# Kernel tuning notes

Measured on AMD Instinct MI355X. Metric: run time of the kernel, lower is better.

The kernel has to match this reference:

```python
import jax, jax.numpy as jnp
import numpy as np

B, D, H, O, E, K = 16384, 128, 512, 128, 8, 2
T = 1.0
EPS = float(np.finfo(float).eps)  # combine() zero-fill epsilon


def cv_squared(v):
    # torch .var() is unbiased (ddof=1)
    return jnp.var(v, ddof=1) / (jnp.mean(v) ** 2 + 1e-10)


def setup_inputs() -> dict:
    key = jax.random.key(0)
    k0, k1, k2, k3, k4, k5 = jax.random.split(key, 6)
    x = jax.random.normal(k0, (B, D), dtype=jnp.float32)
    w_gate = jax.random.normal(k1, (D, E), dtype=jnp.float32) * 0.02
    w1 = jax.random.normal(k2, (E, D, H), dtype=jnp.float32) * (1.0 / np.sqrt(D))
    b1 = jax.random.normal(k3, (E, H), dtype=jnp.float32) * 0.01
    w2 = jax.random.normal(k4, (E, H, O), dtype=jnp.float32) * (1.0 / np.sqrt(H))
    b2 = jax.random.normal(k5, (E, O), dtype=jnp.float32) * 0.01
    return {"x": x, "w_gate": w_gate, "w1": w1, "b1": b1, "w2": w2, "b2": b2}


def reference(x, w_gate, w1, b1, w2, b2):
    # ---- noisy top-k gating (eval mode: clean logits, no noise) ----
    logits = x @ w_gate                                   # [B, E]
    top_logits, top_idx = jax.lax.top_k(logits, K)        # [B, K]
    top_gates = jax.nn.softmax(top_logits / T, axis=-1)   # [B, K]
    gates = jnp.zeros_like(logits).at[jnp.arange(x.shape[0])[:, None], top_idx].set(top_gates)

    importance = gates.sum(0)                              # [E]
    load = (gates > 0).sum(0).astype(jnp.float32)          # [E]
    loss = cv_squared(importance) + cv_squared(load)

    # ---- experts (dense gate-weighted form of dispatch/combine) ----
    # output[b] = Sum_i gates[b,i] * expert_i(x[b]); zero gates contribute nothing,
    # identical math to SparseDispatcher's gather / per-expert MLP / scatter-add.
    h = jax.nn.relu(jnp.einsum('bd,edh->beh', x, w1) + b1[None])   # [B, E, H]
    y_e = jnp.einsum('beh,eho->beo', h, w2) + b2[None]             # [B, E, O]
    y = jnp.einsum('be,beo->bo', gates, y_e)                       # [B, O]
    # combine(): combined[combined == 0] = eps
    y = jnp.where(y == 0, jnp.asarray(EPS, y.dtype), y)
    return y, loss
```

## Files before the change

### kernel.cpp

```cpp
#include <hip/hip_runtime.h>
#include <hip/hip_bf16.h>
#include <math.h>

#define NB 16384
#define ND 128
#define NH 512
#define NO 128
#define NE 8
#define NCH 16
#define EPSF 2.2204460492503131e-16f

using bf16x8 = __attribute__((ext_vector_type(8))) short;
using f32x16 = __attribute__((ext_vector_type(16))) float;
using uint2v = __attribute__((ext_vector_type(2))) unsigned;

#define WS_BLKCNT 0u
#define WS_BLKIMP 8192u
#define WS_TOKID  16384u
#define WS_TOKGG  1064960u
#define WS_XBF    1196032u
#define WS_W1F    5390336u
#define WS_W2F    6438912u
#define WS_YSTAGE 7487488u

__device__ __forceinline__ unsigned f2bf(float f){
  unsigned u = __float_as_uint(f);
  u += 0x7FFFu + ((u >> 16) & 1u);
  return u >> 16;
}
__device__ __forceinline__ unsigned cvtpk(float lo, float hi){
  unsigned r;
  asm("v_cvt_pk_bf16_f32 %0, %1, %2" : "=v"(r) : "v"(lo), "v"(hi));
  return r;
}
__device__ __forceinline__ void gld16(const void* g, void* l){
  __builtin_amdgcn_global_load_lds((const __attribute__((address_space(1))) void*)g,
                                   (__attribute__((address_space(3))) void*)l, 16, 0, 0);
}

__global__ __launch_bounds__(256) void prep_kernel(
    const float* __restrict__ x, const float* __restrict__ wg,
    const float* __restrict__ w1, const float* __restrict__ w2,
    unsigned short* __restrict__ xbf, unsigned short* __restrict__ w1f,
    unsigned short* __restrict__ w2f, int* __restrict__ blk_cnt,
    float* __restrict__ blk_imp, int* __restrict__ tok_ids, float2* __restrict__ tok_gg){
  int bx = blockIdx.x, tid = threadIdx.x;
  if (bx >= 512){
    int u = (bx - 512)*256 + tid;
    int o = u & 127, hb = (u>>7)&3, c = (u>>9)&15, e = u>>13;
    int h0 = c*32 + (hb>>1)*16 + (hb&1)*8;
    const float* src = w2 + (size_t)e*NH*NO + (size_t)h0*NO + o;
    unsigned q[4];
    #pragma unroll
    for (int p = 0; p < 4; ++p)
      q[p] = f2bf(src[(2*p)*NO]) | (f2bf(src[(2*p+1)*NO]) << 16);
    *(uint4*)(w2f + (size_t)u*8) = make_uint4(q[0], q[1], q[2], q[3]);
    return;
  }
  if (bx >= 256){
    int u = (bx - 256)*256 + tid;
    int h32 = u & 31, db = (u>>5)&15, c = (u>>9)&15, e = u>>13;
    int d0 = (db>>1)*16 + (db&1)*8;
    int hg = c*32 + h32;
    const float* src = w1 + (size_t)e*ND*NH + (size_t)d0*NH + hg;
    unsigned q[4];
    #pragma unroll
    for (int p = 0; p < 4; ++p)
      q[p] = f2bf(src[(2*p)*NH]) | (f2bf(src[(2*p+1)*NH]) << 16);
    *(uint4*)(w1f + (size_t)u*8) = make_uint4(q[0], q[1], q[2], q[3]);
    return;
  }
  __shared__ int   lcnt[NE];
  __shared__ float limp[NE];
  if (tid < NE){ lcnt[tid] = 0; limp[tid] = 0.f; }
  __syncthreads();
  int tok  = bx*64 + (tid >> 2);
  int part = tid & 3;
  const float4* xr4 = (const float4*)(x + (size_t)tok*ND);
  double acc[NE];
  #pragma unroll
  for (int e = 0; e < NE; ++e) acc[e] = 0.0;
  #pragma unroll
  for (int j = 0; j < 8; ++j){
    int f4 = part + j*4;
    float4 v = xr4[f4];
    uint2 p;
    p.x = f2bf(v.x) | (f2bf(v.y) << 16);
    p.y = f2bf(v.z) | (f2bf(v.w) << 16);
    *(uint2*)(xbf + (size_t)tok*ND + f4*4) = p;
    const float4* wr = (const float4*)(wg + f4*32);
    float vm[4] = {v.x, v.y, v.z, v.w};
    #pragma unroll
    for (int m = 0; m < 4; ++m){
      float4 wa = wr[2*m], wb = wr[2*m+1];
      double d = (double)vm[m];
      acc[0] += d*(double)wa.x; acc[1] += d*(double)wa.y;
      acc[2] += d*(double)wa.z; acc[3] += d*(double)wa.w;
      acc[4] += d*(double)wb.x; acc[5] += d*(double)wb.y;
      acc[6] += d*(double)wb.z; acc[7] += d*(double)wb.w;
    }
  }
  #pragma unroll
  for (int e = 0; e < NE; ++e){
    acc[e] += __shfl_xor(acc[e], 1);
    acc[e] += __shfl_xor(acc[e], 2);
  }
  if (part == 0){
    int i0 = 0;
    double l0 = acc[0];
    #pragma unroll
    for (int e = 1; e < NE; ++e) if (acc[e] > l0){ l0 = acc[e]; i0 = e; }
    int i1 = (i0 == 0) ? 1 : 0;
    double l1 = acc[i1];
    #pragma unroll
    for (int e = 0; e < NE; ++e) if (e != i0 && acc[e] > l1){ l1 = acc[e]; i1 = e; }
    float e1 = expf((float)(l1 - l0));
    float g0 = 1.0f/(1.0f + e1);
    float g1 = e1/(1.0f + e1);
    int s0 = atomicAdd(&lcnt[i0], 1);
    int s1 = atomicAdd(&lcnt[i1], 1);
    atomicAdd(&limp[i0], g0);
    atomicAdd(&limp[i1], g1);
    tok_gg[tok] = make_float2(g0, g1);
    tok_ids[i0*32768 + bx*128 + s0] = tok;
    tok_ids[i1*32768 + bx*128 + s1] = tok | (1 << 30);
  }
  __syncthreads();
  if (tid < NE){
    blk_cnt[bx*8 + tid] = lcnt[tid];
    blk_imp[bx*8 + tid] = limp[tid];
  }
}

__global__ __launch_bounds__(256) void expert_kernel(
    const unsigned short* __restrict__ xbf, const unsigned short* __restrict__ w1f,
    const unsigned short* __restrict__ w2f, const float* __restrict__ b1,
    const float* __restrict__ b2, const int* __restrict__ blk_cnt,
    const int* __restrict__ tok_ids, const float2* __restrict__ tok_gg,
    unsigned short* __restrict__ ystage){
  __shared__ char L[44032];
  int* cnt_l  = (int*)(L + 32768);
  int* gp     = (int*)(L + 40960);
  int* totl   = (int*)(L + 41984);
  int* tbase  = (int*)(L + 42016);
  int* sl_tok = (int*)(L + 42056);
  int tid = threadIdx.x;
  {
    int4 a = *(const int4*)(blk_cnt + tid*8);
    int4 c = *(const int4*)(blk_cnt + tid*8 + 4);
    cnt_l[0*256+tid]=a.x; cnt_l[1*256+tid]=a.y; cnt_l[2*256+tid]=a.z; cnt_l[3*256+tid]=a.w;
    cnt_l[4*256+tid]=c.x; cnt_l[5*256+tid]=c.y; cnt_l[6*256+tid]=c.z; cnt_l[7*256+tid]=c.w;
  }
  __syncthreads();
  {
    int e8 = tid >> 5, g8 = tid & 31;
    int s8 = 0;
    #pragma unroll
    for (int i = 0; i < 8; ++i) s8 += cnt_l[e8*256 + g8*8 + i];
    gp[tid] = s8;
    __syncthreads();
    #pragma unroll
    for (int st = 1; st < 32; st <<= 1){
      int add = (g8 >= st) ? gp[tid - st] : 0;
      __syncthreads();
      gp[tid] += add;
      __syncthreads();
    }
    if (g8 == 31) totl[e8] = gp[tid];
    __syncthreads();
    if (tid == 0){
      tbase[0] = 0;
      #pragma unroll
      for (int e = 0; e < NE; ++e) tbase[e+1] = tbase[e] + ((totl[e] + 127) >> 7);
    }
    __syncthreads();
  }
  int b = blockIdx.x;
  if (b >= tbase[8]) return;
  int e = 0;
  #pragma unroll
  for (int ee = 1; ee < NE; ++ee) if (tbase[ee] <= b) e = ee;
  int n_e  = totl[e];
  int base = (b - tbase[e])*128;
  if (tid < 128){
    int s = base + tid;
    if (s >= n_e) s = n_e - 1;
    int g = 0;
    #pragma unroll
    for (int st = 16; st; st >>= 1){
      int c = g + st;
      if (c <= 31 && gp[e*32 + c - 1] <= s) g = c;
    }
    int acc2 = g ? gp[e*32 + g - 1] : 0;
    int gb = g*8;
    while (true){
      int c2 = cnt_l[e*256 + gb];
      if (acc2 + c2 > s) break;
      acc2 += c2; ++gb;
    }
    sl_tok[tid] = tok_ids[e*32768 + gb*128 + (s - acc2)];
  }
  __syncthreads();

  int wid = tid >> 6, lane = tid & 63, l31 = lane & 31, hi = lane >> 5;
  char* w1buf = L;
  char* w2buf = L + 16384;
  const char* g1base = (const char*)w1f + (size_t)e*131072;
  const char* g2base = (const char*)w2f + (size_t)e*131072;

  int raw0 = sl_tok[wid*32 + l31];
  int tok0 = raw0 & 0x3FFFFFFF;
  bf16x8 xfrag[8];
  #pragma unroll
  for (int k = 0; k < 8; ++k)
    xfrag[k] = *(const bf16x8*)(xbf + (size_t)tok0*ND + (k*2 + hi)*8);

#define STAGE(c, bsel) do { \
    const char* _g1 = g1base + (size_t)(c)*8192 + wid*1024 + lane*16; \
    const char* _g2 = g2base + (size_t)(c)*8192 + wid*1024 + lane*16; \
    char* _l1 = w1buf + (bsel)*8192 + wid*1024; \
    char* _l2 = w2buf + (bsel)*8192 + wid*1024; \
    _Pragma("unroll") \
    for (int _s = 0; _s < 2; ++_s){ \
      gld16(_g1 + _s*4096, _l1 + _s*4096); \
      gld16(_g2 + _s*4096, _l2 + _s*4096); \
    } \
  } while(0)

  STAGE(0, 0);
  f32x16 yacc[4];
  #pragma unroll
  for (int ot = 0; ot < 4; ++ot)
    #pragma unroll
    for (int i = 0; i < 16; ++i) yacc[ot][i] = 0.f;
  __syncthreads();

  for (int c = 0; c < NCH; ++c){
    int bb = c & 1;
    if (c + 1 < NCH) STAGE(c + 1, bb ^ 1);
    f32x16 hacc;
    #pragma unroll
    for (int i = 0; i < 16; ++i) hacc[i] = 0.f;
    #pragma unroll
    for (int k = 0; k < 8; ++k){
      bf16x8 a = *(const bf16x8*)(w1buf + bb*8192 + (k*2 + hi)*512 + l31*16);
      hacc = __builtin_amdgcn_mfma_f32_32x32x16_bf16(a, xfrag[k], hacc, 0, 0, 0);
    }
    const float4* b1p = (const float4*)(b1 + e*NH + c*32 + hi*4);
    float dv[16];
    #pragma unroll
    for (int g = 0; g < 4; ++g){
      float4 bv = b1p[2*g];
      dv[4*g+0] = fmaxf(hacc[4*g+0] + bv.x, 0.f);
      dv[4*g+1] = fmaxf(hacc[4*g+1] + bv.y, 0.f);
      dv[4*g+2] = fmaxf(hacc[4*g+2] + bv.z, 0.f);
      dv[4*g+3] = fmaxf(hacc[4*g+3] + bv.w, 0.f);
    }
    unsigned A0 = cvtpk(dv[0], dv[1]),   A1 = cvtpk(dv[2], dv[3]);
    unsigned A2 = cvtpk(dv[4], dv[5]),   A3 = cvtpk(dv[6], dv[7]);
    unsigned A4 = cvtpk(dv[8], dv[9]),   A5 = cvtpk(dv[10], dv[11]);
    unsigned A6 = cvtpk(dv[12], dv[13]), A7 = cvtpk(dv[14], dv[15]);
    uint2v r0 = __builtin_amdgcn_permlane32_swap(A0, A2, false, false);
    uint2v r1 = __builtin_amdgcn_permlane32_swap(A1, A3, false, false);
    uint2v r2 = __builtin_amdgcn_permlane32_swap(A4, A6, false, false);
    uint2v r3 = __builtin_amdgcn_permlane32_swap(A5, A7, false, false);
    union { unsigned u[4]; bf16x8 v; } fa, fb;
    fa.u[0] = r0[0]; fa.u[1] = r1[0]; fa.u[2] = r0[1]; fa.u[3] = r1[1];
    fb.u[0] = r2[0]; fb.u[1] = r3[0]; fb.u[2] = r2[1]; fb.u[3] = r3[1];
    bf16x8 aht0 = fa.v, aht1 = fb.v;
    #pragma unroll
    for (int ot = 0; ot < 4; ++ot){
      bf16x8 bf0 = *(const bf16x8*)(w2buf + bb*8192 + hi*2048 + (ot*32 + l31)*16);
      yacc[ot] = __builtin_amdgcn_mfma_f32_32x32x16_bf16(aht0, bf0, yacc[ot], 0, 0, 0);
      bf16x8 bf1 = *(const bf16x8*)(w2buf + bb*8192 + (2 + hi)*2048 + (ot*32 + l31)*16);
      yacc[ot] = __builtin_amdgcn_mfma_f32_32x32x16_bf16(aht1, bf1, yacc[ot], 0, 0, 0);
    }
    __syncthreads();
  }
#undef STAGE
  float b2v[4];
  #pragma unroll
  for (int ot = 0; ot < 4; ++ot) b2v[ot] = b2[e*NO + ot*32 + l31];
  #pragma unroll
  for (int r = 0; r < 16; ++r){
    int row = (r & 3) + 8*(r >> 2) + 4*hi;
    int slot = base + wid*32 + row;
    if (slot < n_e){
      int rw = sl_tok[wid*32 + row];
      int tk = rw & 0x3FFFFFFF, wh = (rw >> 30) & 1;
      float2 gg = tok_gg[tk];
      float g = wh ? gg.y : gg.x;
      unsigned short* dst = ystage + ((size_t)tk*2 + wh)*NO + l31;
      #pragma unroll
      for (int ot = 0; ot < 4; ++ot)
        dst[ot*32] = (unsigned short)f2bf((yacc[ot][r] + b2v[ot]) * g);
    }
  }
}

__global__ __launch_bounds__(256) void combine_kernel(
    const unsigned short* __restrict__ ystage, const int* __restrict__ blk_cnt,
    const float* __restrict__ blk_imp, float* __restrict__ y){
  if (blockIdx.x == 0){
    __shared__ int   scnt[32];
    __shared__ float simp[32];
    int tid = threadIdx.x, lane = tid & 63, wid = tid >> 6;
    int4 ca = *(const int4*)(blk_cnt + tid*8);
    int4 cb = *(const int4*)(blk_cnt + tid*8 + 4);
    float4 ia = *(const float4*)(blk_imp + tid*8);
    float4 ib = *(const float4*)(blk_imp + tid*8 + 4);
    int   cv[8] = {ca.x, ca.y, ca.z, ca.w, cb.x, cb.y, cb.z, cb.w};
    float iv[8] = {ia.x, ia.y, ia.z, ia.w, ib.x, ib.y, ib.z, ib.w};
    #pragma unroll
    for (int e = 0; e < NE; ++e){
      int   rc = cv[e];
      float ri = iv[e];
      #pragma unroll
      for (int st = 1; st < 64; st <<= 1){
        rc += __shfl_xor(rc, st);
        ri += __shfl_xor(ri, st);
      }
      if (lane == 0){ scnt[e*4 + wid] = rc; simp[e*4 + wid] = ri; }
    }
    __syncthreads();
    if (tid == 0){
      double si = 0, sqi = 0, sl = 0, sql = 0;
      #pragma unroll
      for (int e = 0; e < NE; ++e){
        double a = (double)(simp[e*4] + simp[e*4+1] + simp[e*4+2] + simp[e*4+3]);
        double bb = (double)(scnt[e*4] + scnt[e*4+1] + scnt[e*4+2] + scnt[e*4+3]);
        si += a; sqi += a*a; sl += bb; sql += bb*bb;
      }
      double mi = si/8.0, vi = (sqi - 8.0*mi*mi)/7.0;
      double ml = sl/8.0, vl = (sql - 8.0*ml*ml)/7.0;
      y[NB*NO] = (float)(vi/(mi*mi + 1e-10) + vl/(ml*ml + 1e-10));
    }
  }
  int idx = blockIdx.x*256 + threadIdx.x;
  int tk = idx >> 4, q = idx & 15;
  const unsigned short* r0 = ystage + (size_t)tk*256 + q*8;
  uint4 a = *(const uint4*)r0;
  uint4 bq = *(const uint4*)(r0 + 128);
  unsigned aw[4] = {a.x, a.y, a.z, a.w};
  unsigned bw[4] = {bq.x, bq.y, bq.z, bq.w};
  float outs[8];
  #pragma unroll
  for (int i = 0; i < 4; ++i){
    float vlo = __uint_as_float(aw[i] << 16)         + __uint_as_float(bw[i] << 16);
    float vhi = __uint_as_float(aw[i] & 0xFFFF0000u) + __uint_as_float(bw[i] & 0xFFFF0000u);
    outs[2*i]   = (vlo == 0.f) ? EPSF : vlo;
    outs[2*i+1] = (vhi == 0.f) ? EPSF : vhi;
  }
  float4 o0 = {outs[0], outs[1], outs[2], outs[3]};
  float4 o1 = {outs[4], outs[5], outs[6], outs[7]};
  float* dst = y + (size_t)tk*128 + q*8;
  *(float4*)dst     = o0;
  *(float4*)(dst+4) = o1;
}

extern "C" void kernel_launch(void* const* d_in, const int* in_sizes, int n_in,
                              void* d_out, int out_size, void* d_ws, size_t ws_size,
                              hipStream_t stream){
  (void)in_sizes; (void)n_in; (void)out_size; (void)ws_size;
  const float* x  = (const float*)d_in[0];
  const float* wg = (const float*)d_in[1];
  const float* w1 = (const float*)d_in[2];
  const float* b1 = (const float*)d_in[3];
  const float* w2 = (const float*)d_in[4];
  const float* b2 = (const float*)d_in[5];
  float* out = (float*)d_out;
  char* ws = (char*)d_ws;
  int*            blk_cnt = (int*)(ws + WS_BLKCNT);
  float*          blk_imp = (float*)(ws + WS_BLKIMP);
  int*            tok_ids = (int*)(ws + WS_TOKID);
  float2*         tok_gg  = (float2*)(ws + WS_TOKGG);
  unsigned short* xbf     = (unsigned short*)(ws + WS_XBF);
  unsigned short* w1f     = (unsigned short*)(ws + WS_W1F);
  unsigned short* w2f     = (unsigned short*)(ws + WS_W2F);
  unsigned short* ystage  = (unsigned short*)(ws + WS_YSTAGE);

  prep_kernel<<<768, 256, 0, stream>>>(x, wg, w1, w2, xbf, w1f, w2f,
                                       blk_cnt, blk_imp, tok_ids, tok_gg);
  expert_kernel<<<264, 256, 0, stream>>>(xbf, w1f, w2f, b1, b2,
                                         blk_cnt, tok_ids, tok_gg, ystage);
  combine_kernel<<<1024, 256, 0, stream>>>(ystage, blk_cnt, blk_imp, out);
}
```

Baseline: 48.39 us.

## Fuse combine into expert kernel via float atomicAdd into pre-zeroed output

Removes the separate combine kernel and the bf16 staging buffer. The prep kernel now zeroes the output, and the expert kernel atomically adds each gate-weighted expert result straight into the fp32 output. The expert kernel's block 0 also computes the load-balancing loss. This saves one launch and the staging write and read, at the cost of global atomic traffic and an extra zeroing pass. The order of the two per-token additions is now nondeterministic, and the epsilon substitution for exact-zero outputs is dropped.

```diff
diff --git a/kernel.cpp b/kernel.cpp
--- a/kernel.cpp
+++ b/kernel.cpp
@@ -21,7 +21,6 @@
 #define WS_XBF    1196032u
 #define WS_W1F    5390336u
 #define WS_W2F    6438912u
-#define WS_YSTAGE 7487488u
 
 __device__ __forceinline__ unsigned f2bf(float f){
   unsigned u = __float_as_uint(f);
@@ -43,7 +42,8 @@
     const float* __restrict__ w1, const float* __restrict__ w2,
     unsigned short* __restrict__ xbf, unsigned short* __restrict__ w1f,
     unsigned short* __restrict__ w2f, int* __restrict__ blk_cnt,
-    float* __restrict__ blk_imp, int* __restrict__ tok_ids, float2* __restrict__ tok_gg){
+    float* __restrict__ blk_imp, int* __restrict__ tok_ids, float2* __restrict__ tok_gg,
+    float* __restrict__ y){
   int bx = blockIdx.x, tid = threadIdx.x;
   if (bx >= 512){
     int u = (bx - 512)*256 + tid;
@@ -69,6 +69,13 @@
       q[p] = f2bf(src[(2*p)*NH]) | (f2bf(src[(2*p+1)*NH]) << 16);
     *(uint4*)(w1f + (size_t)u*8) = make_uint4(q[0], q[1], q[2], q[3]);
     return;
+  }
+  {
+    float4 z = {0.f, 0.f, 0.f, 0.f};
+    float* yb = y + (size_t)bx*64*NO + tid*32;
+    #pragma unroll
+    for (int i = 0; i < 8; ++i) *(float4*)(yb + i*4) = z;
+    if (bx == 0 && tid == 0) y[NB*NO] = 0.f;
   }
   __shared__ int   lcnt[NE];
   __shared__ float limp[NE];
@@ -136,14 +143,15 @@
     const unsigned short* __restrict__ xbf, const unsigned short* __restrict__ w1f,
     const unsigned short* __restrict__ w2f, const float* __restrict__ b1,
     const float* __restrict__ b2, const int* __restrict__ blk_cnt,
-    const int* __restrict__ tok_ids, const float2* __restrict__ tok_gg,
-    unsigned short* __restrict__ ystage){
+    const float* __restrict__ blk_imp, const int* __restrict__ tok_ids,
+    const float2* __restrict__ tok_gg, float* __restrict__ y){
   __shared__ char L[44032];
   int* cnt_l  = (int*)(L + 32768);
   int* gp     = (int*)(L + 40960);
   int* totl   = (int*)(L + 41984);
   int* tbase  = (int*)(L + 42016);
   int* sl_tok = (int*)(L + 42056);
+  float* simp = (float*)(L + 42568);
   int tid = threadIdx.x;
   {
     int4 a = *(const int4*)(blk_cnt + tid*8);
@@ -177,6 +185,32 @@
   }
   int b = blockIdx.x;
   if (b >= tbase[8]) return;
+  if (b == 0){
+    int lane = tid & 63, wv = tid >> 6;
+    float4 ia = *(const float4*)(blk_imp + tid*8);
+    float4 ib = *(const float4*)(blk_imp + tid*8 + 4);
+    float iv[8] = {ia.x, ia.y, ia.z, ia.w, ib.x, ib.y, ib.z, ib.w};
+    #pragma unroll
+    for (int e2 = 0; e2 < NE; ++e2){
+      float ri = iv[e2];
+      #pragma unroll
+      for (int st = 1; st < 64; st <<= 1) ri += __shfl_xor(ri, st);
+      if (lane == 0) simp[e2*4 + wv] = ri;
+    }
+    __syncthreads();
+    if (tid == 0){
+      double si = 0, sqi = 0, sl = 0, sql = 0;
+      #pragma unroll
+      for (int e2 = 0; e2 < NE; ++e2){
+        double a = (double)(simp[e2*4] + simp[e2*4+1] + simp[e2*4+2] + simp[e2*4+3]);
+        double bb = (double)totl[e2];
+        si += a; sqi += a*a; sl += bb; sql += bb*bb;
+      }
+      double mi = si/8.0, vi = (sqi - 8.0*mi*mi)/7.0;
+      double ml = sl/8.0, vl = (sql - 8.0*ml*ml)/7.0;
+      y[NB*NO] = (float)(vi/(mi*mi + 1e-10) + vl/(ml*ml + 1e-10));
+    }
+  }
   int e = 0;
   #pragma unroll
   for (int ee = 1; ee < NE; ++ee) if (tbase[ee] <= b) e = ee;
@@ -290,72 +324,12 @@
       int tk = rw & 0x3FFFFFFF, wh = (rw >> 30) & 1;
       float2 gg = tok_gg[tk];
       float g = wh ? gg.y : gg.x;
-      unsigned short* dst = ystage + ((size_t)tk*2 + wh)*NO + l31;
+      float* yrow = y + (size_t)tk*NO + l31;
       #pragma unroll
       for (int ot = 0; ot < 4; ++ot)
-        dst[ot*32] = (unsigned short)f2bf((yacc[ot][r] + b2v[ot]) * g);
-    }
-  }
-}
-
-__global__ __launch_bounds__(256) void combine_kernel(
-    const unsigned short* __restrict__ ystage, const int* __restrict__ blk_cnt,
-    const float* __restrict__ blk_imp, float* __restrict__ y){
-  if (blockIdx.x == 0){
-    __shared__ int   scnt[32];
-    __shared__ float simp[32];
-    int tid = threadIdx.x, lane = tid & 63, wid = tid >> 6;
-    int4 ca = *(const int4*)(blk_cnt + tid*8);
-    int4 cb = *(const int4*)(blk_cnt + tid*8 + 4);
-    float4 ia = *(const float4*)(blk_imp + tid*8);
-    float4 ib = *(const float4*)(blk_imp + tid*8 + 4);
-    int   cv[8] = {ca.x, ca.y, ca.z, ca.w, cb.x, cb.y, cb.z, cb.w};
-    float iv[8] = {ia.x, ia.y, ia.z, ia.w, ib.x, ib.y, ib.z, ib.w};
-    #pragma unroll
-    for (int e = 0; e < NE; ++e){
-      int   rc = cv[e];
-      float ri = iv[e];
-      #pragma unroll
-      for (int st = 1; st < 64; st <<= 1){
-        rc += __shfl_xor(rc, st);
-        ri += __shfl_xor(ri, st);
-      }
-      if (lane == 0){ scnt[e*4 + wid] = rc; simp[e*4 + wid] = ri; }
-    }
-    __syncthreads();
-    if (tid == 0){
-      double si = 0, sqi = 0, sl = 0, sql = 0;
-      #pragma unroll
-      for (int e = 0; e < NE; ++e){
-        double a = (double)(simp[e*4] + simp[e*4+1] + simp[e*4+2] + simp[e*4+3]);
-        double bb = (double)(scnt[e*4] + scnt[e*4+1] + scnt[e*4+2] + scnt[e*4+3]);
-        si += a; sqi += a*a; sl += bb; sql += bb*bb;
-      }
-      double mi = si/8.0, vi = (sqi - 8.0*mi*mi)/7.0;
-      double ml = sl/8.0, vl = (sql - 8.0*ml*ml)/7.0;
-      y[NB*NO] = (float)(vi/(mi*mi + 1e-10) + vl/(ml*ml + 1e-10));
-    }
-  }
-  int idx = blockIdx.x*256 + threadIdx.x;
-  int tk = idx >> 4, q = idx & 15;
-  const unsigned short* r0 = ystage + (size_t)tk*256 + q*8;
-  uint4 a = *(const uint4*)r0;
-  uint4 bq = *(const uint4*)(r0 + 128);
-  unsigned aw[4] = {a.x, a.y, a.z, a.w};
-  unsigned bw[4] = {bq.x, bq.y, bq.z, bq.w};
-  float outs[8];
-  #pragma unroll
-  for (int i = 0; i < 4; ++i){
-    float vlo = __uint_as_float(aw[i] << 16)         + __uint_as_float(bw[i] << 16);
-    float vhi = __uint_as_float(aw[i] & 0xFFFF0000u) + __uint_as_float(bw[i] & 0xFFFF0000u);
-    outs[2*i]   = (vlo == 0.f) ? EPSF : vlo;
-    outs[2*i+1] = (vhi == 0.f) ? EPSF : vhi;
-  }
-  float4 o0 = {outs[0], outs[1], outs[2], outs[3]};
-  float4 o1 = {outs[4], outs[5], outs[6], outs[7]};
-  float* dst = y + (size_t)tk*128 + q*8;
-  *(float4*)dst     = o0;
-  *(float4*)(dst+4) = o1;
+        atomicAdd(yrow + ot*32, (yacc[ot][r] + b2v[ot]) * g);
+    }
+  }
 }
 
 extern "C" void kernel_launch(void* const* d_in, const int* in_sizes, int n_in,
@@ -377,11 +351,9 @@
   unsigned short* xbf     = (unsigned short*)(ws + WS_XBF);
   unsigned short* w1f     = (unsigned short*)(ws + WS_W1F);
   unsigned short* w2f     = (unsigned short*)(ws + WS_W2F);
-  unsigned short* ystage  = (unsigned short*)(ws + WS_YSTAGE);
 
   prep_kernel<<<768, 256, 0, stream>>>(x, wg, w1, w2, xbf, w1f, w2f,
-                                       blk_cnt, blk_imp, tok_ids, tok_gg);
+                                       blk_cnt, blk_imp, tok_ids, tok_gg, out);
   expert_kernel<<<264, 256, 0, stream>>>(xbf, w1f, w2f, b1, b2,
-                                         blk_cnt, tok_ids, tok_gg, ystage);
-  combine_kernel<<<1024, 256, 0, stream>>>(ystage, blk_cnt, blk_imp, out);
-}
+                                         blk_cnt, blk_imp, tok_ids, tok_gg, out);
+}
```

Measured after the change: 53.80 us. 11.2% more time.

## Restructure expert kernel into single-wave 64-token blocks with barrier-free pipelining

Applied to the files above, without the earlier changes.

Each expert block becomes a single 64-lane wavefront that handles 64 tokens as two 32-token MFMA groups sharing every weight fragment. The prefix-scan switches from shared-memory scans with block barriers to wave shuffles, and the weight chunks move through a two-deep prefetch controlled by explicit vmcnt waits instead of __syncthreads. b1 is staged in LDS. The launch grows to 520 small blocks, which raises the block count but lowers waves per block. Each wave also stages the full weight set itself, so per-wave load traffic goes up.

```diff
diff --git a/kernel.cpp b/kernel.cpp
--- a/kernel.cpp
+++ b/kernel.cpp
@@ -7,7 +7,6 @@
 #define NH 512
 #define NO 128
 #define NE 8
-#define NCH 16
 #define EPSF 2.2204460492503131e-16f
 
 using bf16x8 = __attribute__((ext_vector_type(8))) short;
@@ -132,58 +131,62 @@
   }
 }
 
-__global__ __launch_bounds__(256) void expert_kernel(
+__global__ __launch_bounds__(64, 1) void expert_kernel(
     const unsigned short* __restrict__ xbf, const unsigned short* __restrict__ w1f,
     const unsigned short* __restrict__ w2f, const float* __restrict__ b1,
     const float* __restrict__ b2, const int* __restrict__ blk_cnt,
     const int* __restrict__ tok_ids, const float2* __restrict__ tok_gg,
     unsigned short* __restrict__ ystage){
-  __shared__ char L[44032];
-  int* cnt_l  = (int*)(L + 32768);
-  int* gp     = (int*)(L + 40960);
-  int* totl   = (int*)(L + 41984);
-  int* tbase  = (int*)(L + 42016);
-  int* sl_tok = (int*)(L + 42056);
-  int tid = threadIdx.x;
-  {
-    int4 a = *(const int4*)(blk_cnt + tid*8);
-    int4 c = *(const int4*)(blk_cnt + tid*8 + 4);
-    cnt_l[0*256+tid]=a.x; cnt_l[1*256+tid]=a.y; cnt_l[2*256+tid]=a.z; cnt_l[3*256+tid]=a.w;
-    cnt_l[4*256+tid]=c.x; cnt_l[5*256+tid]=c.y; cnt_l[6*256+tid]=c.z; cnt_l[7*256+tid]=c.w;
-  }
-  __syncthreads();
-  {
-    int e8 = tid >> 5, g8 = tid & 31;
+  __shared__ char L[35200];
+  char*  wbuf   = L;
+  int*   cnt_l  = (int*)L;
+  int*   gp     = (int*)(L + 8192);
+  int*   sl_tok = (int*)(L + 32768);
+  float* b1s    = (float*)(L + 33024);
+  int*   totl   = (int*)(L + 35072);
+  int*   tbase  = (int*)(L + 35104);
+  int lane = threadIdx.x, l31 = lane & 31, hi = lane >> 5;
+
+  #pragma unroll
+  for (int j = 0; j < 4; ++j){
+    int blk = lane + j*64;
+    int4 a = *(const int4*)(blk_cnt + blk*8);
+    int4 c4 = *(const int4*)(blk_cnt + blk*8 + 4);
+    cnt_l[0*256+blk]=a.x;  cnt_l[1*256+blk]=a.y;  cnt_l[2*256+blk]=a.z;  cnt_l[3*256+blk]=a.w;
+    cnt_l[4*256+blk]=c4.x; cnt_l[5*256+blk]=c4.y; cnt_l[6*256+blk]=c4.z; cnt_l[7*256+blk]=c4.w;
+  }
+  asm volatile("s_waitcnt lgkmcnt(0)" ::: "memory");
+  #pragma unroll
+  for (int p = 0; p < 4; ++p){
+    int e8 = p*2 + hi, g = l31;
     int s8 = 0;
     #pragma unroll
-    for (int i = 0; i < 8; ++i) s8 += cnt_l[e8*256 + g8*8 + i];
-    gp[tid] = s8;
-    __syncthreads();
+    for (int i = 0; i < 8; ++i) s8 += cnt_l[e8*256 + g*8 + i];
+    int pre = s8;
     #pragma unroll
     for (int st = 1; st < 32; st <<= 1){
-      int add = (g8 >= st) ? gp[tid - st] : 0;
-      __syncthreads();
-      gp[tid] += add;
-      __syncthreads();
-    }
-    if (g8 == 31) totl[e8] = gp[tid];
-    __syncthreads();
-    if (tid == 0){
-      tbase[0] = 0;
-      #pragma unroll
-      for (int e = 0; e < NE; ++e) tbase[e+1] = tbase[e] + ((totl[e] + 127) >> 7);
-    }
-    __syncthreads();
-  }
+      int o = __shfl_up(pre, st, 32);
+      if (g >= st) pre += o;
+    }
+    gp[e8*32 + g] = pre;
+    if (g == 31) totl[e8] = pre;
+  }
+  asm volatile("s_waitcnt lgkmcnt(0)" ::: "memory");
+  if (lane == 0){
+    tbase[0] = 0;
+    #pragma unroll
+    for (int e = 0; e < NE; ++e) tbase[e+1] = tbase[e] + ((totl[e] + 63) >> 6);
+  }
+  asm volatile("s_waitcnt lgkmcnt(0)" ::: "memory");
   int b = blockIdx.x;
   if (b >= tbase[8]) return;
   int e = 0;
   #pragma unroll
   for (int ee = 1; ee < NE; ++ee) if (tbase[ee] <= b) e = ee;
   int n_e  = totl[e];
-  int base = (b - tbase[e])*128;
-  if (tid < 128){
-    int s = base + tid;
+  int base = (b - tbase[e])*64;
+  {
+    int s = base + lane;
     if (s >= n_e) s = n_e - 1;
     int g = 0;
     #pragma unroll
@@ -198,104 +201,130 @@
       if (acc2 + c2 > s) break;
       acc2 += c2; ++gb;
     }
-    sl_tok[tid] = tok_ids[e*32768 + gb*128 + (s - acc2)];
-  }
-  __syncthreads();
-
-  int wid = tid >> 6, lane = tid & 63, l31 = lane & 31, hi = lane >> 5;
-  char* w1buf = L;
-  char* w2buf = L + 16384;
+    sl_tok[lane] = tok_ids[e*32768 + gb*128 + (s - acc2)];
+  }
+  asm volatile("s_waitcnt lgkmcnt(0)" ::: "memory");
+  gld16((const char*)(b1 + e*NH) + lane*16, b1s);
+  gld16((const char*)(b1 + e*NH) + 1024 + lane*16, (char*)b1s + 1024);
+  int tokA = sl_tok[l31] & 0x3FFFFFFF;
+  int tokB = sl_tok[32 + l31] & 0x3FFFFFFF;
+  bf16x8 xfA[8], xfB[8];
+  #pragma unroll
+  for (int k = 0; k < 8; ++k){
+    xfA[k] = *(const bf16x8*)(xbf + (size_t)tokA*ND + (k*2 + hi)*8);
+    xfB[k] = *(const bf16x8*)(xbf + (size_t)tokB*ND + (k*2 + hi)*8);
+  }
   const char* g1base = (const char*)w1f + (size_t)e*131072;
   const char* g2base = (const char*)w2f + (size_t)e*131072;
 
-  int raw0 = sl_tok[wid*32 + l31];
-  int tok0 = raw0 & 0x3FFFFFFF;
-  bf16x8 xfrag[8];
-  #pragma unroll
-  for (int k = 0; k < 8; ++k)
-    xfrag[k] = *(const bf16x8*)(xbf + (size_t)tok0*ND + (k*2 + hi)*8);
-
 #define STAGE(c, bsel) do { \
-    const char* _g1 = g1base + (size_t)(c)*8192 + wid*1024 + lane*16; \
-    const char* _g2 = g2base + (size_t)(c)*8192 + wid*1024 + lane*16; \
-    char* _l1 = w1buf + (bsel)*8192 + wid*1024; \
-    char* _l2 = w2buf + (bsel)*8192 + wid*1024; \
+    const char* _g1 = g1base + (size_t)(c)*8192 + lane*16; \
+    const char* _g2 = g2base + (size_t)(c)*8192 + lane*16; \
+    char* _l1 = wbuf + (bsel)*16384; \
+    char* _l2 = wbuf + (bsel)*16384 + 8192; \
     _Pragma("unroll") \
-    for (int _s = 0; _s < 2; ++_s){ \
-      gld16(_g1 + _s*4096, _l1 + _s*4096); \
-      gld16(_g2 + _s*4096, _l2 + _s*4096); \
+    for (int _i = 0; _i < 8; ++_i){ \
+      gld16(_g1 + _i*1024, _l1 + _i*1024); \
+      gld16(_g2 + _i*1024, _l2 + _i*1024); \
     } \
   } while(0)
 
+#define REPACK(dv, out0, out1) do { \
+    unsigned A0=cvtpk(dv[0],dv[1]),   A1=cvtpk(dv[2],dv[3]); \
+    unsigned A2=cvtpk(dv[4],dv[5]),   A3=cvtpk(dv[6],dv[7]); \
+    unsigned A4=cvtpk(dv[8],dv[9]),   A5=cvtpk(dv[10],dv[11]); \
+    unsigned A6=cvtpk(dv[12],dv[13]), A7=cvtpk(dv[14],dv[15]); \
+    uint2v r0 = __builtin_amdgcn_permlane32_swap(A0, A2, false, false); \
+    uint2v r1 = __builtin_amdgcn_permlane32_swap(A1, A3, false, false); \
+    uint2v r2 = __builtin_amdgcn_permlane32_swap(A4, A6, false, false); \
+    uint2v r3 = __builtin_amdgcn_permlane32_swap(A5, A7, false, false); \
+    union { unsigned u[4]; bf16x8 v; } fa, fb; \
+    fa.u[0]=r0[0]; fa.u[1]=r1[0]; fa.u[2]=r0[1]; fa.u[3]=r1[1]; \
+    fb.u[0]=r2[0]; fb.u[1]=r3[0]; fb.u[2]=r2[1]; fb.u[3]=r3[1]; \
+    out0 = fa.v; out1 = fb.v; \
+  } while(0)
+
   STAGE(0, 0);
-  f32x16 yacc[4];
+  STAGE(1, 1);
+  f32x16 yA[4], yB[4];
   #pragma unroll
   for (int ot = 0; ot < 4; ++ot)
     #pragma unroll
-    for (int i = 0; i < 16; ++i) yacc[ot][i] = 0.f;
-  __syncthreads();
-
-  for (int c = 0; c < NCH; ++c){
-    int bb = c & 1;
-    if (c + 1 < NCH) STAGE(c + 1, bb ^ 1);
-    f32x16 hacc;
-    #pragma unroll
-    for (int i = 0; i < 16; ++i) hacc[i] = 0.f;
+    for (int i = 0; i < 16; ++i){ yA[ot][i] = 0.f; yB[ot][i] = 0.f; }
+
+  #pragma unroll
+  for (int c = 0; c < 16; ++c){
+    if (c < 14) asm volatile("s_waitcnt vmcnt(16)" ::: "memory");
+    else        asm volatile("s_waitcnt vmcnt(0)"  ::: "memory");
+    __builtin_amdgcn_sched_barrier(0);
+    const char* w1c = wbuf + (c & 1)*16384;
+    const char* w2c = wbuf + (c & 1)*16384 + 8192;
+    f32x16 hA, hB;
+    #pragma unroll
+    for (int i = 0; i < 16; ++i){ hA[i] = 0.f; hB[i] = 0.f; }
     #pragma unroll
     for (int k = 0; k < 8; ++k){
-      bf16x8 a = *(const bf16x8*)(w1buf + bb*8192 + (k*2 + hi)*512 + l31*16);
-      hacc = __builtin_amdgcn_mfma_f32_32x32x16_bf16(a, xfrag[k], hacc, 0, 0, 0);
-    }
-    const float4* b1p = (const float4*)(b1 + e*NH + c*32 + hi*4);
-    float dv[16];
+      bf16x8 a = *(const bf16x8*)(w1c + (k*2 + hi)*512 + l31*16);
+      hA = __builtin_amdgcn_mfma_f32_32x32x16_bf16(a, xfA[k], hA, 0, 0, 0);
+      hB = __builtin_amdgcn_mfma_f32_32x32x16_bf16(a, xfB[k], hB, 0, 0, 0);
+    }
+    float dvA[16], dvB[16];
     #pragma unroll
     for (int g = 0; g < 4; ++g){
-      float4 bv = b1p[2*g];
-      dv[4*g+0] = fmaxf(hacc[4*g+0] + bv.x, 0.f);
-      dv[4*g+1] = fmaxf(hacc[4*g+1] + bv.y, 0.f);
-      dv[4*g+2] = fmaxf(hacc[4*g+2] + bv.z, 0.f);
-      dv[4*g+3] = fmaxf(hacc[4*g+3] + bv.w, 0.f);
-    }
-    unsigned A0 = cvtpk(dv[0], dv[1]),   A1 = cvtpk(dv[2], dv[3]);
-    unsigned A2 = cvtpk(dv[4], dv[5]),   A3 = cvtpk(dv[6], dv[7]);
-    unsigned A4 = cvtpk(dv[8], dv[9]),   A5 = cvtpk(dv[10], dv[11]);
-    unsigned A6 = cvtpk(dv[12], dv[13]), A7 = cvtpk(dv[14], dv[15]);
-    uint2v r0 = __builtin_amdgcn_permlane32_swap(A0, A2, false, false);
-    uint2v r1 = __builtin_amdgcn_permlane32_swap(A1, A3, false, false);
-    uint2v r2 = __builtin_amdgcn_permlane32_swap(A4, A6, false, false);
-    uint2v r3 = __builtin_amdgcn_permlane32_swap(A5, A7, false, false);
-    union { unsigned u[4]; bf16x8 v; } fa, fb;
-    fa.u[0] = r0[0]; fa.u[1] = r1[0]; fa.u[2] = r0[1]; fa.u[3] = r1[1];
-    fb.u[0] = r2[0]; fb.u[1] = r3[0]; fb.u[2] = r2[1]; fb.u[3] = r3[1];
-    bf16x8 aht0 = fa.v, aht1 = fb.v;
+      float4 bv = *(const float4*)(b1s + c*32 + hi*4 + g*8);
+      dvA[4*g+0] = fmaxf(hA[4*g+0] + bv.x, 0.f);
+      dvA[4*g+1] = fmaxf(hA[4*g+1] + bv.y, 0.f);
+      dvA[4*g+2] = fmaxf(hA[4*g+2] + bv.z, 0.f);
+      dvA[4*g+3] = fmaxf(hA[4*g+3] + bv.w, 0.f);
+      dvB[4*g+0] = fmaxf(hB[4*g+0] + bv.x, 0.f);
+      dvB[4*g+1] = fmaxf(hB[4*g+1] + bv.y, 0.f);
+      dvB[4*g+2] = fmaxf(hB[4*g+2] + bv.z, 0.f);
+      dvB[4*g+3] = fmaxf(hB[4*g+3] + bv.w, 0.f);
+    }
+    bf16x8 ahA0, ahA1, ahB0, ahB1;
+    REPACK(dvA, ahA0, ahA1);
+    REPACK(dvB, ahB0, ahB1);
     #pragma unroll
     for (int ot = 0; ot < 4; ++ot){
-      bf16x8 bf0 = *(const bf16x8*)(w2buf + bb*8192 + hi*2048 + (ot*32 + l31)*16);
-      yacc[ot] = __builtin_amdgcn_mfma_f32_32x32x16_bf16(aht0, bf0, yacc[ot], 0, 0, 0);
-      bf16x8 bf1 = *(const bf16x8*)(w2buf + bb*8192 + (2 + hi)*2048 + (ot*32 + l31)*16);
-      yacc[ot] = __builtin_amdgcn_mfma_f32_32x32x16_bf16(aht1, bf1, yacc[ot], 0, 0, 0);
-    }
-    __syncthreads();
+      bf16x8 bf0 = *(const bf16x8*)(w2c + hi*2048 + (ot*32 + l31)*16);
+      bf16x8 bf1 = *(const bf16x8*)(w2c + (2 + hi)*2048 + (ot*32 + l31)*16);
+      yA[ot] = __builtin_amdgcn_mfma_f32_32x32x16_bf16(ahA0, bf0, yA[ot], 0, 0, 0);
+      yA[ot] = __builtin_amdgcn_mfma_f32_32x32x16_bf16(ahA1, bf1, yA[ot], 0, 0, 0);
+      yB[ot] = __builtin_amdgcn_mfma_f32_32x32x16_bf16(ahB0, bf0, yB[ot], 0, 0, 0);
+      yB[ot] = __builtin_amdgcn_mfma_f32_32x32x16_bf16(ahB1, bf1, yB[ot], 0, 0, 0);
+    }
+    if (c + 2 < 16){
+      asm volatile("s_waitcnt lgkmcnt(0)" ::: "memory");
+      __builtin_amdgcn_sched_barrier(0);
+      STAGE(c + 2, c & 1);
+    }
   }
 #undef STAGE
+#undef REPACK
+
   float b2v[4];
   #pragma unroll
   for (int ot = 0; ot < 4; ++ot) b2v[ot] = b2[e*NO + ot*32 + l31];
-  #pragma unroll
-  for (int r = 0; r < 16; ++r){
-    int row = (r & 3) + 8*(r >> 2) + 4*hi;
-    int slot = base + wid*32 + row;
-    if (slot < n_e){
-      int rw = sl_tok[wid*32 + row];
-      int tk = rw & 0x3FFFFFFF, wh = (rw >> 30) & 1;
-      float2 gg = tok_gg[tk];
-      float g = wh ? gg.y : gg.x;
-      unsigned short* dst = ystage + ((size_t)tk*2 + wh)*NO + l31;
-      #pragma unroll
-      for (int ot = 0; ot < 4; ++ot)
-        dst[ot*32] = (unsigned short)f2bf((yacc[ot][r] + b2v[ot]) * g);
-    }
-  }
+#define EPI(G, Y) do { \
+    _Pragma("unroll") \
+    for (int r = 0; r < 16; ++r){ \
+      int row = (r & 3) + 8*(r >> 2) + 4*hi; \
+      int slot = base + (G)*32 + row; \
+      if (slot < n_e){ \
+        int rw = sl_tok[(G)*32 + row]; \
+        int tk = rw & 0x3FFFFFFF, wh = (rw >> 30) & 1; \
+        float2 gg = tok_gg[tk]; \
+        float gsc = wh ? gg.y : gg.x; \
+        unsigned short* dst = ystage + ((size_t)tk*2 + wh)*NO + l31; \
+        _Pragma("unroll") \
+        for (int ot = 0; ot < 4; ++ot) \
+          dst[ot*32] = (unsigned short)f2bf((Y[ot][r] + b2v[ot]) * gsc); \
+      } \
+    } \
+  } while(0)
+  EPI(0, yA);
+  EPI(1, yB);
+#undef EPI
 }
 
 __global__ __launch_bounds__(256) void combine_kernel(
@@ -381,7 +410,7 @@
 
   prep_kernel<<<768, 256, 0, stream>>>(x, wg, w1, w2, xbf, w1f, w2f,
                                        blk_cnt, blk_imp, tok_ids, tok_gg);
-  expert_kernel<<<264, 256, 0, stream>>>(xbf, w1f, w2f, b1, b2,
-                                         blk_cnt, tok_ids, tok_gg, ystage);
+  expert_kernel<<<520, 64, 0, stream>>>(xbf, w1f, w2f, b1, b2,
+                                        blk_cnt, tok_ids, tok_gg, ystage);
   combine_kernel<<<1024, 256, 0, stream>>>(ystage, blk_cnt, blk_imp, out);
 }
```

Result: slower. 56.01 us (+15.8%).

## Split expert MLP over hidden-dim quarters and output halves with more blocks

Applied to the files above, without the earlier changes.

The expert kernel now splits each 64-token tile across 4 blocks, one per quarter of the hidden dimension, and splits each block's warps over two token halves and two output halves. Weights are read straight from global memory instead of being double-buffered through LDS, and the LDS-barrier prefix scan becomes a wave shuffle scan. Each block writes a bf16 partial, with the bias pre-scaled by 0.25, and combine sums 8 partials per token. This targets poor occupancy from only 264 blocks, but it adds extra partial-sum traffic and more bf16 rounding error.

```diff
diff --git a/kernel.cpp b/kernel.cpp
--- a/kernel.cpp
+++ b/kernel.cpp
@@ -7,7 +7,6 @@
 #define NH 512
 #define NO 128
 #define NE 8
-#define NCH 16
 #define EPSF 2.2204460492503131e-16f
 
 using bf16x8 = __attribute__((ext_vector_type(8))) short;
@@ -21,7 +20,7 @@
 #define WS_XBF    1196032u
 #define WS_W1F    5390336u
 #define WS_W2F    6438912u
-#define WS_YSTAGE 7487488u
+#define WS_YST4   7487488u
 
 __device__ __forceinline__ unsigned f2bf(float f){
   unsigned u = __float_as_uint(f);
@@ -32,10 +31,6 @@
   unsigned r;
   asm("v_cvt_pk_bf16_f32 %0, %1, %2" : "=v"(r) : "v"(lo), "v"(hi));
   return r;
-}
-__device__ __forceinline__ void gld16(const void* g, void* l){
-  __builtin_amdgcn_global_load_lds((const __attribute__((address_space(1))) void*)g,
-                                   (__attribute__((address_space(3))) void*)l, 16, 0, 0);
 }
 
 __global__ __launch_bounds__(256) void prep_kernel(
@@ -132,24 +127,22 @@
   }
 }
 
-__global__ __launch_bounds__(256) void expert_kernel(
+__global__ __launch_bounds__(256, 4) void expert_kernel(
     const unsigned short* __restrict__ xbf, const unsigned short* __restrict__ w1f,
     const unsigned short* __restrict__ w2f, const float* __restrict__ b1,
     const float* __restrict__ b2, const int* __restrict__ blk_cnt,
     const int* __restrict__ tok_ids, const float2* __restrict__ tok_gg,
     unsigned short* __restrict__ ystage){
-  __shared__ char L[44032];
-  int* cnt_l  = (int*)(L + 32768);
-  int* gp     = (int*)(L + 40960);
-  int* totl   = (int*)(L + 41984);
-  int* tbase  = (int*)(L + 42016);
-  int* sl_tok = (int*)(L + 42056);
+  __shared__ int cnt_l[NE*256];
+  __shared__ int gp[256];
+  __shared__ int totl[NE];
+  __shared__ int sl_tok[64];
   int tid = threadIdx.x;
   {
     int4 a = *(const int4*)(blk_cnt + tid*8);
-    int4 c = *(const int4*)(blk_cnt + tid*8 + 4);
-    cnt_l[0*256+tid]=a.x; cnt_l[1*256+tid]=a.y; cnt_l[2*256+tid]=a.z; cnt_l[3*256+tid]=a.w;
-    cnt_l[4*256+tid]=c.x; cnt_l[5*256+tid]=c.y; cnt_l[6*256+tid]=c.z; cnt_l[7*256+tid]=c.w;
+    int4 c4 = *(const int4*)(blk_cnt + tid*8 + 4);
+    cnt_l[0*256+tid]=a.x;  cnt_l[1*256+tid]=a.y;  cnt_l[2*256+tid]=a.z;  cnt_l[3*256+tid]=a.w;
+    cnt_l[4*256+tid]=c4.x; cnt_l[5*256+tid]=c4.y; cnt_l[6*256+tid]=c4.z; cnt_l[7*256+tid]=c4.w;
   }
   __syncthreads();
   {
@@ -157,33 +150,32 @@
     int s8 = 0;
     #pragma unroll
     for (int i = 0; i < 8; ++i) s8 += cnt_l[e8*256 + g8*8 + i];
-    gp[tid] = s8;
-    __syncthreads();
+    int pre = s8;
     #pragma unroll
     for (int st = 1; st < 32; st <<= 1){
-      int add = (g8 >= st) ? gp[tid - st] : 0;
-      __syncthreads();
-      gp[tid] += add;
-      __syncthreads();
-    }
-    if (g8 == 31) totl[e8] = gp[tid];
-    __syncthreads();
-    if (tid == 0){
-      tbase[0] = 0;
-      #pragma unroll
-      for (int e = 0; e < NE; ++e) tbase[e+1] = tbase[e] + ((totl[e] + 127) >> 7);
-    }
-    __syncthreads();
-  }
-  int b = blockIdx.x;
-  if (b >= tbase[8]) return;
+      int o = __shfl_up(pre, st, 32);
+      if (g8 >= st) pre += o;
+    }
+    gp[tid] = pre;
+    if (g8 == 31) totl[e8] = pre;
+  }
+  __syncthreads();
+  int tb[9];
+  tb[0] = 0;
+  #pragma unroll
+  for (int e2 = 0; e2 < NE; ++e2) tb[e2+1] = tb[e2] + ((totl[e2] + 63) >> 6);
+  int tile_g = blockIdx.x >> 2, q = blockIdx.x & 3;
+  if (tile_g >= tb[8]) return;
   int e = 0;
   #pragma unroll
-  for (int ee = 1; ee < NE; ++ee) if (tbase[ee] <= b) e = ee;
+  for (int ee = 1; ee < NE; ++ee) if (tb[ee] <= tile_g) e = ee;
   int n_e  = totl[e];
-  int base = (b - tbase[e])*128;
-  if (tid < 128){
-    int s = base + tid;
+  int base = (tile_g - tb[e])*64;
+  int lane = tid & 63, wid = tid >> 6, l31 = lane & 31, hi = lane >> 5;
+  int t = wid & 1, oh = wid >> 1;
+  int raw;
+  {
+    int s = base + t*32 + l31;
     if (s >= n_e) s = n_e - 1;
     int g = 0;
     #pragma unroll
@@ -198,55 +190,39 @@
       if (acc2 + c2 > s) break;
       acc2 += c2; ++gb;
     }
-    sl_tok[tid] = tok_ids[e*32768 + gb*128 + (s - acc2)];
-  }
-  __syncthreads();
-
-  int wid = tid >> 6, lane = tid & 63, l31 = lane & 31, hi = lane >> 5;
-  char* w1buf = L;
-  char* w2buf = L + 16384;
-  const char* g1base = (const char*)w1f + (size_t)e*131072;
-  const char* g2base = (const char*)w2f + (size_t)e*131072;
-
-  int raw0 = sl_tok[wid*32 + l31];
-  int tok0 = raw0 & 0x3FFFFFFF;
-  bf16x8 xfrag[8];
+    raw = tok_ids[e*32768 + gb*128 + (s - acc2)];
+  }
+  if (oh == 0) sl_tok[t*32 + l31] = raw;
+  __syncthreads();
+
+  int tok0 = raw & 0x3FFFFFFF;
+  bf16x8 xf[8];
   #pragma unroll
   for (int k = 0; k < 8; ++k)
-    xfrag[k] = *(const bf16x8*)(xbf + (size_t)tok0*ND + (k*2 + hi)*8);
-
-#define STAGE(c, bsel) do { \
-    const char* _g1 = g1base + (size_t)(c)*8192 + wid*1024 + lane*16; \
-    const char* _g2 = g2base + (size_t)(c)*8192 + wid*1024 + lane*16; \
-    char* _l1 = w1buf + (bsel)*8192 + wid*1024; \
-    char* _l2 = w2buf + (bsel)*8192 + wid*1024; \
-    _Pragma("unroll") \
-    for (int _s = 0; _s < 2; ++_s){ \
-      gld16(_g1 + _s*4096, _l1 + _s*4096); \
-      gld16(_g2 + _s*4096, _l2 + _s*4096); \
-    } \
-  } while(0)
-
-  STAGE(0, 0);
-  f32x16 yacc[4];
-  #pragma unroll
-  for (int ot = 0; ot < 4; ++ot)
+    xf[k] = *(const bf16x8*)(xbf + (size_t)tok0*ND + (k*2 + hi)*8);
+  const char* w1e = (const char*)w1f + (size_t)e*131072;
+  const char* w2e = (const char*)w2f + (size_t)e*131072;
+
+  f32x16 yacc[2];
+  #pragma unroll
+  for (int ot = 0; ot < 2; ++ot)
     #pragma unroll
     for (int i = 0; i < 16; ++i) yacc[ot][i] = 0.f;
-  __syncthreads();
-
-  for (int c = 0; c < NCH; ++c){
-    int bb = c & 1;
-    if (c + 1 < NCH) STAGE(c + 1, bb ^ 1);
+
+  #pragma unroll
+  for (int c = 0; c < 4; ++c){
+    int c32 = q*4 + c;
+    const char* w1c = w1e + (size_t)c32*8192;
+    const char* w2c = w2e + (size_t)c32*8192;
     f32x16 hacc;
     #pragma unroll
     for (int i = 0; i < 16; ++i) hacc[i] = 0.f;
     #pragma unroll
     for (int k = 0; k < 8; ++k){
-      bf16x8 a = *(const bf16x8*)(w1buf + bb*8192 + (k*2 + hi)*512 + l31*16);
-      hacc = __builtin_amdgcn_mfma_f32_32x32x16_bf16(a, xfrag[k], hacc, 0, 0, 0);
-    }
-    const float4* b1p = (const float4*)(b1 + e*NH + c*32 + hi*4);
+      bf16x8 a = *(const bf16x8*)(w1c + (k*2 + hi)*512 + l31*16);
+      hacc = __builtin_amdgcn_mfma_f32_32x32x16_bf16(a, xf[k], hacc, 0, 0, 0);
+    }
+    const float4* b1p = (const float4*)(b1 + e*NH + c32*32 + hi*4);
     float dv[16];
     #pragma unroll
     for (int g = 0; g < 4; ++g){
@@ -269,31 +245,32 @@
     fb.u[0] = r2[0]; fb.u[1] = r3[0]; fb.u[2] = r2[1]; fb.u[3] = r3[1];
     bf16x8 aht0 = fa.v, aht1 = fb.v;
     #pragma unroll
-    for (int ot = 0; ot < 4; ++ot){
-      bf16x8 bf0 = *(const bf16x8*)(w2buf + bb*8192 + hi*2048 + (ot*32 + l31)*16);
+    for (int ot = 0; ot < 2; ++ot){
+      int oidx = ((oh*2 + ot)*32 + l31)*16;
+      bf16x8 bf0 = *(const bf16x8*)(w2c + hi*2048 + oidx);
+      bf16x8 bf1 = *(const bf16x8*)(w2c + (2 + hi)*2048 + oidx);
       yacc[ot] = __builtin_amdgcn_mfma_f32_32x32x16_bf16(aht0, bf0, yacc[ot], 0, 0, 0);
-      bf16x8 bf1 = *(const bf16x8*)(w2buf + bb*8192 + (2 + hi)*2048 + (ot*32 + l31)*16);
       yacc[ot] = __builtin_amdgcn_mfma_f32_32x32x16_bf16(aht1, bf1, yacc[ot], 0, 0, 0);
     }
-    __syncthreads();
-  }
-#undef STAGE
-  float b2v[4];
-  #pragma unroll
-  for (int ot = 0; ot < 4; ++ot) b2v[ot] = b2[e*NO + ot*32 + l31];
+  }
+
+  float b2q = 0.25f;
+  float b2v[2];
+  #pragma unroll
+  for (int ot = 0; ot < 2; ++ot) b2v[ot] = b2[e*NO + (oh*2 + ot)*32 + l31]*b2q;
   #pragma unroll
   for (int r = 0; r < 16; ++r){
     int row = (r & 3) + 8*(r >> 2) + 4*hi;
-    int slot = base + wid*32 + row;
+    int slot = base + t*32 + row;
     if (slot < n_e){
-      int rw = sl_tok[wid*32 + row];
+      int rw = sl_tok[t*32 + row];
       int tk = rw & 0x3FFFFFFF, wh = (rw >> 30) & 1;
       float2 gg = tok_gg[tk];
-      float g = wh ? gg.y : gg.x;
-      unsigned short* dst = ystage + ((size_t)tk*2 + wh)*NO + l31;
+      float gsc = wh ? gg.y : gg.x;
+      unsigned short* dst = ystage + (((size_t)tk*2 + wh)*4 + q)*NO + l31;
       #pragma unroll
-      for (int ot = 0; ot < 4; ++ot)
-        dst[ot*32] = (unsigned short)f2bf((yacc[ot][r] + b2v[ot]) * g);
+      for (int ot = 0; ot < 2; ++ot)
+        dst[(oh*2 + ot)*32] = (unsigned short)f2bf((yacc[ot][r] + b2v[ot]) * gsc);
     }
   }
 }
@@ -337,23 +314,24 @@
     }
   }
   int idx = blockIdx.x*256 + threadIdx.x;
-  int tk = idx >> 4, q = idx & 15;
-  const unsigned short* r0 = ystage + (size_t)tk*256 + q*8;
-  uint4 a = *(const uint4*)r0;
-  uint4 bq = *(const uint4*)(r0 + 128);
-  unsigned aw[4] = {a.x, a.y, a.z, a.w};
-  unsigned bw[4] = {bq.x, bq.y, bq.z, bq.w};
-  float outs[8];
-  #pragma unroll
-  for (int i = 0; i < 4; ++i){
-    float vlo = __uint_as_float(aw[i] << 16)         + __uint_as_float(bw[i] << 16);
-    float vhi = __uint_as_float(aw[i] & 0xFFFF0000u) + __uint_as_float(bw[i] & 0xFFFF0000u);
-    outs[2*i]   = (vlo == 0.f) ? EPSF : vlo;
-    outs[2*i+1] = (vhi == 0.f) ? EPSF : vhi;
-  }
-  float4 o0 = {outs[0], outs[1], outs[2], outs[3]};
-  float4 o1 = {outs[4], outs[5], outs[6], outs[7]};
-  float* dst = y + (size_t)tk*128 + q*8;
+  int tk = idx >> 4, oc = idx & 15;
+  const unsigned short* rbase = ystage + (size_t)tk*8*NO + oc*8;
+  float s[8] = {0.f,0.f,0.f,0.f,0.f,0.f,0.f,0.f};
+  #pragma unroll
+  for (int wq = 0; wq < 8; ++wq){
+    uint4 a = *(const uint4*)(rbase + (size_t)wq*NO);
+    unsigned aw[4] = {a.x, a.y, a.z, a.w};
+    #pragma unroll
+    for (int i = 0; i < 4; ++i){
+      s[2*i]   += __uint_as_float(aw[i] << 16);
+      s[2*i+1] += __uint_as_float(aw[i] & 0xFFFF0000u);
+    }
+  }
+  #pragma unroll
+  for (int i = 0; i < 8; ++i) s[i] = (s[i] == 0.f) ? EPSF : s[i];
+  float4 o0 = {s[0], s[1], s[2], s[3]};
+  float4 o1 = {s[4], s[5], s[6], s[7]};
+  float* dst = y + (size_t)tk*128 + oc*8;
   *(float4*)dst     = o0;
   *(float4*)(dst+4) = o1;
 }
@@ -377,11 +355,11 @@
   unsigned short* xbf     = (unsigned short*)(ws + WS_XBF);
   unsigned short* w1f     = (unsigned short*)(ws + WS_W1F);
   unsigned short* w2f     = (unsigned short*)(ws + WS_W2F);
-  unsigned short* ystage  = (unsigned short*)(ws + WS_YSTAGE);
+  unsigned short* ystage  = (unsigned short*)(ws + WS_YST4);
 
   prep_kernel<<<768, 256, 0, stream>>>(x, wg, w1, w2, xbf, w1f, w2f,
                                        blk_cnt, blk_imp, tok_ids, tok_gg);
-  expert_kernel<<<264, 256, 0, stream>>>(xbf, w1f, w2f, b1, b2,
-                                         blk_cnt, tok_ids, tok_gg, ystage);
+  expert_kernel<<<2080, 256, 0, stream>>>(xbf, w1f, w2f, b1, b2,
+                                          blk_cnt, tok_ids, tok_gg, ystage);
   combine_kernel<<<1024, 256, 0, stream>>>(ystage, blk_cnt, blk_imp, out);
 }
```

Measured after the change: 67.40 us, median of 2. 39.3% more time.
